# Kernel optimization log

Measured on AMD Instinct MI355X. Metric: run time of the kernel, lower is better.

Reference implementation:

```python
import jax, jax.numpy as jnp
import numpy as np

B, S, D = 8, 8192, 64
N_HASHES = 8
BUCKET_SIZE = 64
N_BUCKETS = S // BUCKET_SIZE  # 128
SELF_ATTN_VALUE = -5e4  # torch reformer TOKEN_SELF_ATTN_VALUE


def setup_inputs() -> dict:
    key = jax.random.key(0)
    k1, k2, k3 = jax.random.split(key, 3)
    qk = jax.random.normal(k1, (B, S, D), dtype=jnp.float32)
    v = jax.random.normal(k2, (B, S, D), dtype=jnp.float32)
    # LSH random rotations: (dim, n_hashes, n_buckets // 2), shared across batch/heads
    rotations = jax.random.normal(k3, (D, N_HASHES, N_BUCKETS // 2), dtype=jnp.float32)
    return {"qk": qk, "v": v, "rotations": rotations, "query_len": S}


def _look_one_back(x):
    # concatenate each chunk with the preceding chunk (wrapping) along the kv axis
    x_extra = jnp.concatenate([x[:, -1:], x[:, :-1]], axis=1)
    return jnp.concatenate([x, x_extra], axis=2)


def _lsh_bucketed_dots(qk, v, rotations):
    batch, seqlen, dim = qk.shape
    n_buckets = seqlen // BUCKET_SIZE
    # --- hash vectors: rotate, concat with negation, argmax -> bucket ids ---
    rotated = jnp.einsum('btf,fhi->bhti', qk, rotations)           # (B, H, S, nb/2)
    rotated = jnp.concatenate([rotated, -rotated], axis=-1)        # (B, H, S, nb)
    buckets = jnp.argmax(rotated, axis=-1)                         # (B, H, S) int
    offsets = (jnp.arange(N_HASHES) * n_buckets)[None, :, None]    # disjoint per round
    buckets = (buckets + offsets).reshape(batch, -1)               # (B, H*S)

    # --- stable bucket sort via composite key (all keys unique) ---
    ticker = jnp.arange(N_HASHES * seqlen)[None, :]                # (1, H*S)
    buckets_and_t = seqlen * buckets + (ticker % seqlen)
    sticker = jnp.argsort(buckets_and_t, axis=-1)                  # sort permutation
    undo_sort = jnp.argsort(sticker, axis=-1)                      # inverse permutation
    st = sticker % seqlen                                          # original token ids

    # --- gather tokens into bucket order ---
    sqk = jnp.take_along_axis(qk, st[..., None], axis=1)           # (B, H*S, D)
    sv = jnp.take_along_axis(v, st[..., None], axis=1)

    n_chunks = N_HASHES * n_buckets
    bq_t = st.reshape(batch, n_chunks, BUCKET_SIZE)                # (B, C, bs)
    bqk = sqk.reshape(batch, n_chunks, BUCKET_SIZE, dim)
    bv = sv.reshape(batch, n_chunks, BUCKET_SIZE, dim)

    bq = bqk
    bk = bqk / (jnp.linalg.norm(bqk, axis=-1, keepdims=True) + 1e-6)  # unit-length keys

    bk = _look_one_back(bk)       # (B, C, 2*bs, D)
    bv = _look_one_back(bv)
    bkv_t = _look_one_back(bq_t)  # (B, C, 2*bs)

    dots = jnp.einsum('buie,buje->buij', bq, bk) * (dim ** -0.5)   # (B, C, bs, 2*bs)
    self_mask = bq_t[:, :, :, None] == bkv_t[:, :, None, :]
    dots = jnp.where(self_mask, SELF_ATTN_VALUE, dots)
    return dots, undo_sort, bv


def reference(qk, v, rotations, query_len):
    batch, seqlen, dim = qk.shape
    dots, undo_sort, bv = _lsh_bucketed_dots(qk, v, rotations)
    dots_logsumexp = jax.nn.logsumexp(dots, axis=-1, keepdims=True)
    p = jnp.exp(dots - dots_logsumexp)                             # per-bucket softmax
    bo = jnp.einsum('buij,buje->buie', p, bv)                      # (B, C, bs, D)
    so = bo.reshape(batch, -1, dim)                                # (B, H*S, D)
    slogits = dots_logsumexp.reshape(batch, -1)                    # (B, H*S)
    # undo the bucket sort
    o = jnp.take_along_axis(so, undo_sort[..., None], axis=1)
    logits = jnp.take_along_axis(slogits, undo_sort, axis=1)
    o = o.reshape(batch, N_HASHES, seqlen, dim)[:, :, :query_len]
    logits = logits.reshape(batch, N_HASHES, seqlen, 1)[:, :, :query_len]
    # combine across hash rounds, weighted by per-round logsumexp
    probs = jnp.exp(logits - jax.nn.logsumexp(logits, axis=1, keepdims=True))
    out = jnp.sum(o * probs, axis=1)                               # (B, query_len, D)
    return out
```

## Files before the change

kernel.cpp:

```cpp
#include <hip/hip_runtime.h>
#include <math.h>

#define B_  8
#define S_  8192
#define D_  64
#define H_  8
#define NB_ 128
#define NC_ 1024
#define REP_CAP 65536
#define T2_ 2e-3f

typedef _Float16 f16x8 __attribute__((ext_vector_type(8)));
typedef _Float16 f16x2 __attribute__((ext_vector_type(2)));
typedef float    f32x4 __attribute__((ext_vector_type(4)));
typedef unsigned int uint_;

#define MFMA16(A, Bv, C) __builtin_amdgcn_mfma_f32_16x16x32_f16(A, Bv, C, 0, 0, 0)

__global__ __launch_bounds__(256) void rot_prep_kernel(
    const float* __restrict__ rot, _Float16* __restrict__ rotHi,
    _Float16* __restrict__ rotLo, float* __restrict__ rotT,
    int* __restrict__ cnt)
{
  __shared__ float rs[64 * 64];
  const int tid = threadIdx.x, h = blockIdx.x;
  if (h == 0 && tid == 0) *cnt = 0;
#pragma unroll
  for (int it = 0; it < 16; ++it) {
    const int f = it * 4 + (tid >> 6), i = tid & 63;
    rs[f * 64 + i] = rot[f * 512 + h * 64 + i];
  }
  __syncthreads();
  const int i = tid & 63, grp = tid >> 6;
  _Float16 hi[16], lo[16];
  float tf[16];
#pragma unroll
  for (int ff = 0; ff < 16; ++ff) {
    const float x = rs[(grp * 16 + ff) * 64 + i];
    tf[ff] = x;
    hi[ff] = (_Float16)x;
    lo[ff] = (_Float16)(x - (float)hi[ff]);
  }
  f16x8* dH = (f16x8*)(rotHi + h * 4096 + i * 64 + grp * 16);
  f16x8* dL = (f16x8*)(rotLo + h * 4096 + i * 64 + grp * 16);
  dH[0] = ((f16x8*)hi)[0]; dH[1] = ((f16x8*)hi)[1];
  dL[0] = ((f16x8*)lo)[0]; dL[1] = ((f16x8*)lo)[1];
  float4* dT = (float4*)(rotT + h * 4096 + i * 64 + grp * 16);
#pragma unroll
  for (int k = 0; k < 4; ++k) dT[k] = ((float4*)tf)[k];
}

__global__ __launch_bounds__(256) void hash_kernel(
    const float* __restrict__ qk, const float* __restrict__ v,
    const _Float16* __restrict__ rotHi, const _Float16* __restrict__ rotLo,
    _Float16* __restrict__ q16, _Float16* __restrict__ kn16,
    _Float16* __restrict__ v16,
    int* __restrict__ bucket, int* __restrict__ cnt, int2* __restrict__ list)
{
  __shared__ float rs[64 * 68];
  __shared__ _Float16 rH[64 * 72];
  __shared__ _Float16 rL[64 * 72];
  const int tid  = threadIdx.x;
  const int b    = blockIdx.x & 7;
  const int tile = blockIdx.x >> 3;
  const int lane = tid & 63, w = tid >> 6;
  const int m16  = lane & 15, qd = lane >> 4;

  {
    const int r = tid >> 2, qu = tid & 3;
    const int gt = b * S_ + tile * 64 + r;
    const size_t off = (size_t)gt * 64 + qu * 16;
    float x[16];
#pragma unroll
    for (int k = 0; k < 4; ++k) ((float4*)x)[k] = ((const float4*)(qk + off))[k];
#pragma unroll
    for (int k = 0; k < 4; ++k)
      *(float4*)(rs + r * 68 + qu * 16 + k * 4) = ((float4*)x)[k];
    float ss = 0.f;
#pragma unroll
    for (int k = 0; k < 16; ++k) ss = fmaf(x[k], x[k], ss);
    ss += __shfl_xor(ss, 1); ss += __shfl_xor(ss, 2);
    const float inv = 0.125f / (sqrtf(ss) + 1e-6f);
    f16x8 qh[2], kn[2];
#pragma unroll
    for (int j = 0; j < 16; ++j) {
      qh[j >> 3][j & 7] = (_Float16)x[j];
      kn[j >> 3][j & 7] = (_Float16)(x[j] * inv);
    }
    ((f16x8*)(q16  + off))[0] = qh[0]; ((f16x8*)(q16  + off))[1] = qh[1];
    ((f16x8*)(kn16 + off))[0] = kn[0]; ((f16x8*)(kn16 + off))[1] = kn[1];
    float y[16];
#pragma unroll
    for (int k = 0; k < 4; ++k) ((float4*)y)[k] = ((const float4*)(v + off))[k];
    f16x8 vv[2];
#pragma unroll
    for (int j = 0; j < 16; ++j) vv[j >> 3][j & 7] = (_Float16)y[j];
    ((f16x8*)(v16 + off))[0] = vv[0]; ((f16x8*)(v16 + off))[1] = vv[1];
  }
  __syncthreads();

  const int t = tile * 64 + w * 16 + m16;
  f16x8 BH0, BH1, BL0, BL1;
  {
    const float* srcl = rs + (w * 16 + m16) * 68 + 8 * qd;
    float x[16];
    ((float4*)x)[0] = *(const float4*)(srcl);
    ((float4*)x)[1] = *(const float4*)(srcl + 4);
    ((float4*)x)[2] = *(const float4*)(srcl + 32);
    ((float4*)x)[3] = *(const float4*)(srcl + 36);
#pragma unroll
    for (int j = 0; j < 8; ++j) {
      const _Float16 h0 = (_Float16)x[j];
      BH0[j] = h0; BL0[j] = (_Float16)(x[j] - (float)h0);
      const _Float16 h1 = (_Float16)x[j + 8];
      BH1[j] = h1; BL1[j] = (_Float16)(x[j + 8] - (float)h1);
    }
  }
  const int srow = tid >> 2, scol = (tid & 3) * 16;
  const uint_ qd16 = (uint_)(qd << 4);

  f16x8 cH0, cH1, cL0, cL1;
  {
    const _Float16* gH = rotHi + srow * 64 + scol;
    const _Float16* gL = rotLo + srow * 64 + scol;
    cH0 = ((const f16x8*)gH)[0]; cH1 = ((const f16x8*)gH)[1];
    cL0 = ((const f16x8*)gL)[0]; cL1 = ((const f16x8*)gL)[1];
  }

#pragma unroll 1
  for (int h = 0; h < 8; ++h) {
    __syncthreads();
    f16x8 nH0, nH1, nL0, nL1;
    if (h < 7) {
      const _Float16* gH = rotHi + (h + 1) * 4096 + srow * 64 + scol;
      const _Float16* gL = rotLo + (h + 1) * 4096 + srow * 64 + scol;
      nH0 = ((const f16x8*)gH)[0]; nH1 = ((const f16x8*)gH)[1];
      nL0 = ((const f16x8*)gL)[0]; nL1 = ((const f16x8*)gL)[1];
    }
    *(f16x8*)(rH + srow * 72 + scol)     = cH0;
    *(f16x8*)(rH + srow * 72 + scol + 8) = cH1;
    *(f16x8*)(rL + srow * 72 + scol)     = cL0;
    *(f16x8*)(rL + srow * 72 + scol + 8) = cL1;
    __syncthreads();

    f32x4 acc[4];
#pragma unroll
    for (int mt = 0; mt < 4; ++mt) acc[mt] = (f32x4){0.f, 0.f, 0.f, 0.f};
#pragma unroll
    for (int mt = 0; mt < 4; ++mt) {
      const _Float16* aH = rH + (16 * mt + m16) * 72 + 8 * qd;
      const _Float16* aL = rL + (16 * mt + m16) * 72 + 8 * qd;
      const f16x8 AH0 = *(const f16x8*)aH;
      const f16x8 AH1 = *(const f16x8*)(aH + 32);
      const f16x8 AL0 = *(const f16x8*)aL;
      const f16x8 AL1 = *(const f16x8*)(aL + 32);
      acc[mt] = MFMA16(AH0, BH0, acc[mt]);
      acc[mt] = MFMA16(AH1, BH1, acc[mt]);
      acc[mt] = MFMA16(AH0, BL0, acc[mt]);
      acc[mt] = MFMA16(AH1, BL1, acc[mt]);
      acc[mt] = MFMA16(AL0, BH0, acc[mt]);
      acc[mt] = MFMA16(AL1, BH1, acc[mt]);
    }

    float v1M = -1e30f, v2M = -1e30f, v1m = 1e30f, v2m = 1e30f;
#pragma unroll
    for (int mt = 0; mt < 4; ++mt)
#pragma unroll
      for (int rg = 0; rg < 4; ++rg) {
        uint_ u = __float_as_uint(acc[mt][rg]);
        u = (u & 0xFFFFFFC0u) | qd16 | (uint_)((mt << 2) | rg);
        const float xk = __uint_as_float(u);
        v2M = __builtin_amdgcn_fmed3f(v1M, v2M, xk);
        v1M = fmaxf(v1M, xk);
        v2m = __builtin_amdgcn_fmed3f(v1m, v2m, xk);
        v1m = fminf(v1m, xk);
      }
#pragma unroll
    for (int off = 16; off <= 32; off <<= 1) {
      const float o1M = __shfl_xor(v1M, off), o2M = __shfl_xor(v2M, off);
      v2M = __builtin_amdgcn_fmed3f(v1M, o1M, fmaxf(v2M, o2M));
      v1M = fmaxf(v1M, o1M);
      const float o1m = __shfl_xor(v1m, off), o2m = __shfl_xor(v2m, off);
      v2m = __builtin_amdgcn_fmed3f(v1m, o1m, fminf(v2m, o2m));
      v1m = fminf(v1m, o1m);
    }
    if (qd == 0) {
      const uint_ cM = __float_as_uint(v1M) & 63u;
      const uint_ cm = __float_as_uint(v1m) & 63u;
      const int ixM = 16 * (int)((cM >> 2) & 3u) + 4 * (int)(cM >> 4) + (int)(cM & 3u);
      const int ixm = 16 * (int)((cm >> 2) & 3u) + 4 * (int)(cm >> 4) + (int)(cm & 3u);
      const int bkt = (v1M >= -v1m) ? ixM : 64 + ixm;
      bucket[((size_t)(b * 8 + h)) * S_ + t] = bkt;
      const bool flag = ((v1M - v2M) < T2_) | ((v2m - v1m) < T2_) |
                        (fabsf(v1M + v1m) < T2_);
      if (flag) {
        const int s = atomicAdd(cnt, 1);
        if (s < REP_CAP) list[s] = make_int2(b * 8 + h, t);
      }
    }
    cH0 = nH0; cH1 = nH1; cL0 = nL0; cL1 = nL1;
  }
}

__global__ __launch_bounds__(256) void repair_kernel(
    const float* __restrict__ qk, const float* __restrict__ rotT,
    const int* __restrict__ cnt, const int2* __restrict__ list,
    int* __restrict__ bucket)
{
  const int n = min(*cnt, REP_CAP);
  const int lane = threadIdx.x & 63;
  const int wid  = (blockIdx.x * 256 + threadIdx.x) >> 6;
  const int nw   = gridDim.x * 4;
  for (int idx = wid; idx < n; idx += nw) {
    const int bh = list[idx].x, t = list[idx].y;
    const int b = bh >> 3, hh = bh & 7;
    const float* qrow = qk + ((size_t)b * S_ + t) * D_;
    const float* rcol = rotT + hh * 4096 + lane * 64;
    double acc = 0.0;
#pragma unroll
    for (int f0 = 0; f0 < 64; f0 += 4) {
      const float4 rq = *(const float4*)(qrow + f0);
      const float4 rc = *(const float4*)(rcol + f0);
      acc = fma((double)rq.x, (double)rc.x, acc);
      acc = fma((double)rq.y, (double)rc.y, acc);
      acc = fma((double)rq.z, (double)rc.z, acc);
      acc = fma((double)rq.w, (double)rc.w, acc);
    }
    double vM = acc; int iM = lane;
    double vm = acc; int im = lane;
#pragma unroll
    for (int off = 32; off >= 1; off >>= 1) {
      const double voM = __shfl_xor(vM, off); const int ioM = __shfl_xor(iM, off);
      if (voM > vM || (voM == vM && ioM < iM)) { vM = voM; iM = ioM; }
      const double vom = __shfl_xor(vm, off); const int iom = __shfl_xor(im, off);
      if (vom < vm || (vom == vm && iom < im)) { vm = vom; im = iom; }
    }
    if (lane == 0) {
      const int bkt = (vM >= -vm) ? iM : 64 + im;
      bucket[(size_t)bh * S_ + t] = bkt;
    }
  }
}

__global__ __launch_bounds__(1024) void sort_kernel(
    const int* __restrict__ bucket, int* __restrict__ st)
{
  __shared__ uint_ hist32[128 * 67];
  __shared__ unsigned short lb[S_];
  __shared__ int off[128];
  __shared__ int wtot;
  unsigned short* hist16 = (unsigned short*)hist32;
  const int tid = threadIdx.x;
  const int bh  = blockIdx.x;
  const size_t base = (size_t)bh * S_;
  const int lane = tid & 63;
  const unsigned long long ltmask = (1ull << lane) - 1ull;

#pragma unroll
  for (int k = 0; k < 9; ++k) {
    const int i = k * 1024 + tid;
    if (i < 128 * 67) hist32[i] = 0;
  }
  __syncthreads();

  int rl[8];
#pragma unroll
  for (int k = 0; k < 8; ++k) {
    const int t = k * 1024 + tid;
    const int bk = bucket[base + t];
    lb[t] = (unsigned short)bk;
    unsigned long long same = ~0ull;
#pragma unroll
    for (int bit = 0; bit < 7; ++bit) {
      const unsigned long long m = __ballot((bk >> bit) & 1);
      same &= ((bk >> bit) & 1) ? m : ~m;
    }
    rl[k] = __popcll(same & ltmask);
    if ((same & ltmask) == 0ull)
      hist16[bk * 134 + (t >> 6)] = (unsigned short)__popcll(same);
  }
  __syncthreads();

  int s = 0;
  if (tid < 128) {
    const uint_* row = hist32 + tid * 67;
#pragma unroll
    for (int g2 = 0; g2 < 64; ++g2) {
      const uint_ wv = row[g2];
      s += (int)((wv & 0xFFFFu) + (wv >> 16));
    }
  }
  int x = s;
#pragma unroll
  for (int d = 1; d < 64; d <<= 1) {
    const int y = __shfl_up(x, d);
    if (lane >= d) x += y;
  }
  if (tid == 63) wtot = x;
  __syncthreads();
  if (tid < 128) {
    if (tid >= 64) x += wtot;
    off[tid] = x - s;
  }
  __syncthreads();

  if (tid < 128) {
    int run = off[tid];
    unsigned short* rowp = hist16 + tid * 134;
#pragma unroll
    for (int g = 0; g < 128; ++g) {
      const int cg = rowp[g];
      rowp[g] = (unsigned short)run;
      run += cg;
    }
  }
  __syncthreads();

  const int b = bh >> 3, h = bh & 7;
  const size_t stb = (size_t)b * (H_ * S_) + (size_t)h * S_;
#pragma unroll
  for (int k = 0; k < 8; ++k) {
    const int t = k * 1024 + tid;
    const int bk = (int)lb[t];
    const int gb = (int)hist16[bk * 134 + (t >> 6)];
    st[stb + gb + rl[k]] = t;
  }
}

__global__ __launch_bounds__(256, 8) void attn_kernel(
    const _Float16* __restrict__ q16, const _Float16* __restrict__ kn16,
    const _Float16* __restrict__ v16, const int* __restrict__ st,
    _Float16* __restrict__ so, float* __restrict__ slog)
{
  __shared__ _Float16 smem[128 * 72];
  __shared__ __align__(16) int sIds[128];

  const int tid = threadIdx.x;
  const int b   = blockIdx.x & 7;
  const int c   = blockIdx.x >> 3;
  const int cm1 = (c + NC_ - 1) & (NC_ - 1);
  const size_t bst = (size_t)b * (H_ * S_);
  const size_t row0 = bst + (size_t)c * 64;
  const size_t row1 = bst + (size_t)cm1 * 64;

  const int lane = tid & 63;
  const int w    = tid >> 6;
  const int m16  = lane & 15;
  const int qd   = lane >> 4;

  if (tid < 128) sIds[tid] = (tid < 64) ? st[row0 + tid] : st[row1 + tid - 64];

  const int rid = st[row0 + 16 * w + m16];
  f16x8 q0, q1;
  {
    const _Float16* qp = q16 + ((size_t)b * S_ + rid) * 64 + 8 * qd;
    q0 = *(const f16x8*)qp;
    q1 = *(const f16x8*)(qp + 32);
  }

  const int r = tid >> 2, qu = tid & 3;
  {
    const int tokA = st[row0 + r];
    const int tokB = st[row1 + r];
    const f16x8* ska = (const f16x8*)(kn16 + ((size_t)b * S_ + tokA) * 64 + qu * 16);
    const f16x8* skb = (const f16x8*)(kn16 + ((size_t)b * S_ + tokB) * 64 + qu * 16);
    *(f16x8*)(smem + r * 72 + qu * 16)            = ska[0];
    *(f16x8*)(smem + r * 72 + qu * 16 + 8)        = ska[1];
    *(f16x8*)(smem + (64 + r) * 72 + qu * 16)     = skb[0];
    *(f16x8*)(smem + (64 + r) * 72 + qu * 16 + 8) = skb[1];
  }
  __syncthreads();

  f32x4 acc[8];
#pragma unroll
  for (int jt = 0; jt < 8; ++jt) acc[jt] = (f32x4){0.f, 0.f, 0.f, 0.f};

  __builtin_amdgcn_s_setprio(1);
#pragma unroll
  for (int jt = 0; jt < 8; ++jt) {
    const _Float16* krow = smem + (16 * jt + m16) * 72;
    const f16x8 kb0 = *(const f16x8*)(krow + 8 * qd);
    const f16x8 kb1 = *(const f16x8*)(krow + 32 + 8 * qd);
    acc[jt] = MFMA16(kb0, q0, acc[jt]);
    acc[jt] = MFMA16(kb1, q1, acc[jt]);
  }
  __builtin_amdgcn_s_setprio(0);

  float m = -1e30f;
#pragma unroll
  for (int jt = 0; jt < 8; ++jt) {
    const int4 cid = *(const int4*)(sIds + 16 * jt + 4 * qd);
    float x;
    x = acc[jt][0]; if (cid.x == rid) x = -5e4f; acc[jt][0] = x; m = fmaxf(m, x);
    x = acc[jt][1]; if (cid.y == rid) x = -5e4f; acc[jt][1] = x; m = fmaxf(m, x);
    x = acc[jt][2]; if (cid.z == rid) x = -5e4f; acc[jt][2] = x; m = fmaxf(m, x);
    x = acc[jt][3]; if (cid.w == rid) x = -5e4f; acc[jt][3] = x; m = fmaxf(m, x);
  }
  m = fmaxf(m, __shfl_xor(m, 16));
  m = fmaxf(m, __shfl_xor(m, 32));
  float sum = 0.f;
#pragma unroll
  for (int jt = 0; jt < 8; ++jt)
#pragma unroll
    for (int rg = 0; rg < 4; ++rg) {
      const float e = __expf(acc[jt][rg] - m);
      acc[jt][rg] = e;
      sum += e;
    }
  sum += __shfl_xor(sum, 16);
  sum += __shfl_xor(sum, 32);
  const float rinv = 1.f / sum;

  const int hh = c >> 7;
  const size_t hb = ((size_t)(b * 8 + hh)) * S_;
  if (qd == 0) slog[hb + rid] = m + __logf(sum);

  f16x8 pa[4];
#pragma unroll
  for (int s = 0; s < 4; ++s)
#pragma unroll
    for (int j = 0; j < 8; ++j)
      pa[s][j] = (_Float16)acc[2 * s + (j >> 2)][j & 3];

  const int c0 = 2 * r;
  const int k0 = 32 * (c0 >> 5) + 16 * ((c0 >> 2) & 1) + 4 * ((c0 >> 3) & 3) + (c0 & 3);
  const int tok0 = sIds[k0], tok1 = sIds[k0 + 1];
  f16x8 va[2], vb[2];
  {
    const f16x8* s0 = (const f16x8*)(v16 + ((size_t)b * S_ + tok0) * 64 + qu * 16);
    const f16x8* s1 = (const f16x8*)(v16 + ((size_t)b * S_ + tok1) * 64 + qu * 16);
    va[0] = s0[0]; va[1] = s0[1];
    vb[0] = s1[0]; vb[1] = s1[1];
  }
  __syncthreads();

  {
    const int swz = (qu << 3) ^ ((qu & 1) << 5);
    _Float16* dst = smem + (c0 ^ swz);
#pragma unroll
    for (int jj = 0; jj < 16; ++jj) {
      const int d = 16 * qu + jj;
      f16x2 pk; pk[0] = va[jj >> 3][jj & 7]; pk[1] = vb[jj >> 3][jj & 7];
      *(f16x2*)(dst + d * 136) = pk;
    }
  }
  __syncthreads();

  f32x4 oacc[4];
#pragma unroll
  for (int dt = 0; dt < 4; ++dt) oacc[dt] = (f32x4){0.f, 0.f, 0.f, 0.f};
  __builtin_amdgcn_s_setprio(1);
#pragma unroll
  for (int s = 0; s < 4; ++s) {
#pragma unroll
    for (int dt = 0; dt < 4; ++dt) {
      const _Float16* vp = smem + (16 * dt + m16) * 136
                         + 32 * (s ^ (dt & 1)) + 8 * (qd ^ dt);
      const f16x8 bv = *(const f16x8*)(vp);
      oacc[dt] = MFMA16(pa[s], bv, oacc[dt]);
    }
  }
  __builtin_amdgcn_s_setprio(0);

  float rin[4];
#pragma unroll
  for (int rg = 0; rg < 4; ++rg) rin[rg] = __shfl(rinv, 4 * qd + rg);

  __syncthreads();
#pragma unroll
  for (int dt = 0; dt < 4; ++dt)
#pragma unroll
    for (int rg = 0; rg < 4; ++rg)
      smem[(16 * w + 4 * qd + rg) * 72 + 16 * dt + m16] =
          (_Float16)(oacc[dt][rg] * rin[rg]);
  __syncthreads();

  {
    const int tok = sIds[r];
    const f16x8* srcp = (const f16x8*)(smem + r * 72 + qu * 16);
    const f16x8 o0 = srcp[0], o1 = srcp[1];
    f16x8* dstp = (f16x8*)(so + (hb + tok) * 64 + qu * 16);
    dstp[0] = o0; dstp[1] = o1;
  }
}

__global__ __launch_bounds__(256) void combine_kernel(
    const _Float16* __restrict__ so, const float* __restrict__ slog,
    float* __restrict__ out)
{
  const int blk = blockIdx.x;
  const int b   = blk & 7;
  const int t   = (blk >> 3) * 32 + (threadIdx.x >> 3);
  const int oct = threadIdx.x & 7;
  const size_t base8 = (size_t)(b * 8) * S_ + t;

  float l[8];
#pragma unroll
  for (int h = 0; h < 8; ++h) l[h] = slog[base8 + (size_t)h * S_];
  float m = l[0];
#pragma unroll
  for (int h = 1; h < 8; ++h) m = fmaxf(m, l[h]);
  float wv[8], W = 0.f;
#pragma unroll
  for (int h = 0; h < 8; ++h) { wv[h] = expf(l[h] - m); W += wv[h]; }
  const float iW = 1.f / W;

  float acc[8] = {0.f, 0.f, 0.f, 0.f, 0.f, 0.f, 0.f, 0.f};
#pragma unroll
  for (int h = 0; h < 8; ++h) {
    const f16x8 vv = *(const f16x8*)(so + (base8 + (size_t)h * S_) * 64 + oct * 8);
#pragma unroll
    for (int j = 0; j < 8; ++j) acc[j] = fmaf(wv[h], (float)vv[j], acc[j]);
  }
  float4 o0, o1;
  o0.x = acc[0] * iW; o0.y = acc[1] * iW; o0.z = acc[2] * iW; o0.w = acc[3] * iW;
  o1.x = acc[4] * iW; o1.y = acc[5] * iW; o1.z = acc[6] * iW; o1.w = acc[7] * iW;
  float4* dst = (float4*)(out + ((size_t)b * S_ + t) * 64 + oct * 8);
  dst[0] = o0; dst[1] = o1;
}

extern "C" void kernel_launch(void* const* d_in, const int* in_sizes, int n_in,
                              void* d_out, int out_size, void* d_ws, size_t ws_size,
                              hipStream_t stream)
{
  const float* qk  = (const float*)d_in[0];
  const float* v   = (const float*)d_in[1];
  const float* rot = (const float*)d_in[2];
  float* out = (float*)d_out;

  char* ws = (char*)d_ws;
  const size_t MB = 1ull << 20, KB = 1024;
  int*      bucket = (int*)      (ws + 0 * MB);
  int*      st     = (int*)      (ws + 2 * MB);
  float*    slog   = (float*)    (ws + 4 * MB);
  _Float16* q16    = (_Float16*) (ws + 8 * MB);
  _Float16* kn16   = (_Float16*) (ws + 16 * MB);
  _Float16* v16    = (_Float16*) (ws + 24 * MB);
  _Float16* rotHi  = (_Float16*) (ws + 32 * MB);
  _Float16* rotLo  = (_Float16*) (ws + 32 * MB + 64 * KB);
  int*      cnt    = (int*)      (ws + 32 * MB + 128 * KB);
  int2*     list   = (int2*)     (ws + 32 * MB + 192 * KB);
  float*    rotT   = (float*)    (ws + 32 * MB + 768 * KB);
  _Float16* so     = (_Float16*) (ws + 33 * MB);
  if (ws_size < 98 * MB) return;

  hipLaunchKernelGGL(rot_prep_kernel, dim3(8),         dim3(256),  0, stream,
                     rot, rotHi, rotLo, rotT, cnt);
  hipLaunchKernelGGL(hash_kernel,     dim3(8 * 128),   dim3(256),  0, stream,
                     qk, v, rotHi, rotLo, q16, kn16, v16, bucket, cnt, list);
  hipLaunchKernelGGL(repair_kernel,   dim3(256),       dim3(256),  0, stream,
                     qk, rotT, cnt, list, bucket);
  hipLaunchKernelGGL(sort_kernel,     dim3(64),        dim3(1024), 0, stream,
                     bucket, st);
  hipLaunchKernelGGL(attn_kernel,     dim3(B_ * NC_),  dim3(256),  0, stream,
                     q16, kn16, v16, st, so, slog);
  hipLaunchKernelGGL(combine_kernel,  dim3(B_ * S_ * 8 / 256), dim3(256), 0, stream,
                     so, slog, out);
}
```

Baseline: 177.6 us.

## Fuse bucket repair into sort kernel and rework attention output stores

Removes the separate repair kernel launch. Each sort block now scans the flagged-token list, picks out the entries for its own (batch, hash) row, and recomputes those buckets in double precision before sorting. The attention kernel's scatter of outputs to the sorted buffer now uses 8 threads per row over two halves with nontemporal 16-byte stores. The fused scan makes every one of the 64 sort blocks read the whole list serially and adds work at the start of sort, in exchange for one fewer launch.

Result: slower. 215.4 us (+21.3%).

```diff
diff --git a/kernel.cpp b/kernel.cpp
--- a/kernel.cpp
+++ b/kernel.cpp
@@ -202,48 +202,10 @@
   }
 }
 
-__global__ __launch_bounds__(256) void repair_kernel(
+__global__ __launch_bounds__(1024) void sort_kernel(
     const float* __restrict__ qk, const float* __restrict__ rotT,
     const int* __restrict__ cnt, const int2* __restrict__ list,
-    int* __restrict__ bucket)
-{
-  const int n = min(*cnt, REP_CAP);
-  const int lane = threadIdx.x & 63;
-  const int wid  = (blockIdx.x * 256 + threadIdx.x) >> 6;
-  const int nw   = gridDim.x * 4;
-  for (int idx = wid; idx < n; idx += nw) {
-    const int bh = list[idx].x, t = list[idx].y;
-    const int b = bh >> 3, hh = bh & 7;
-    const float* qrow = qk + ((size_t)b * S_ + t) * D_;
-    const float* rcol = rotT + hh * 4096 + lane * 64;
-    double acc = 0.0;
-#pragma unroll
-    for (int f0 = 0; f0 < 64; f0 += 4) {
-      const float4 rq = *(const float4*)(qrow + f0);
-      const float4 rc = *(const float4*)(rcol + f0);
-      acc = fma((double)rq.x, (double)rc.x, acc);
-      acc = fma((double)rq.y, (double)rc.y, acc);
-      acc = fma((double)rq.z, (double)rc.z, acc);
-      acc = fma((double)rq.w, (double)rc.w, acc);
-    }
-    double vM = acc; int iM = lane;
-    double vm = acc; int im = lane;
-#pragma unroll
-    for (int off = 32; off >= 1; off >>= 1) {
-      const double voM = __shfl_xor(vM, off); const int ioM = __shfl_xor(iM, off);
-      if (voM > vM || (voM == vM && ioM < iM)) { vM = voM; iM = ioM; }
-      const double vom = __shfl_xor(vm, off); const int iom = __shfl_xor(im, off);
-      if (vom < vm || (vom == vm && iom < im)) { vm = vom; im = iom; }
-    }
-    if (lane == 0) {
-      const int bkt = (vM >= -vm) ? iM : 64 + im;
-      bucket[(size_t)bh * S_ + t] = bkt;
-    }
-  }
-}
-
-__global__ __launch_bounds__(1024) void sort_kernel(
-    const int* __restrict__ bucket, int* __restrict__ st)
+    int* __restrict__ bucket, int* __restrict__ st)
 {
   __shared__ uint_ hist32[128 * 67];
   __shared__ unsigned short lb[S_];
@@ -256,6 +218,50 @@
   const int lane = tid & 63;
   const unsigned long long ltmask = (1ull << lane) - 1ull;
 
+  {
+    const int n = min(*cnt, REP_CAP);
+    const int b = bh >> 3, hh = bh & 7;
+    for (int base_i = 0; base_i < n; base_i += 1024) {
+      const int idx = base_i + tid;
+      int match = 0, ty = 0;
+      if (idx < n) {
+        const int2 e = list[idx];
+        ty = e.y;
+        match = (e.x == bh);
+      }
+      unsigned long long mm = __ballot(match);
+      while (mm) {
+        const int src = (int)__builtin_ctzll(mm); mm &= mm - 1;
+        const int t = __shfl(ty, src);
+        const float* qrow = qk + ((size_t)b * S_ + t) * D_;
+        const float* rcol = rotT + hh * 4096 + lane * 64;
+        double acc = 0.0;
+#pragma unroll
+        for (int f0 = 0; f0 < 64; f0 += 4) {
+          const float4 rq = *(const float4*)(qrow + f0);
+          const float4 rc = *(const float4*)(rcol + f0);
+          acc = fma((double)rq.x, (double)rc.x, acc);
+          acc = fma((double)rq.y, (double)rc.y, acc);
+          acc = fma((double)rq.z, (double)rc.z, acc);
+          acc = fma((double)rq.w, (double)rc.w, acc);
+        }
+        double vM = acc; int iM = lane;
+        double vm = acc; int im = lane;
+#pragma unroll
+        for (int o = 32; o >= 1; o >>= 1) {
+          const double voM = __shfl_xor(vM, o); const int ioM = __shfl_xor(iM, o);
+          if (voM > vM || (voM == vM && ioM < iM)) { vM = voM; iM = ioM; }
+          const double vom = __shfl_xor(vm, o); const int iom = __shfl_xor(im, o);
+          if (vom < vm || (vom == vm && iom < im)) { vm = vom; im = iom; }
+        }
+        if (lane == 0) {
+          const int bkt = (vM >= -vm) ? iM : 64 + im;
+          bucket[(size_t)bh * S_ + t] = bkt;
+        }
+      }
+    }
+  }
+
 #pragma unroll
   for (int k = 0; k < 9; ++k) {
     const int i = k * 1024 + tid;
@@ -476,11 +482,14 @@
   __syncthreads();
 
   {
-    const int tok = sIds[r];
-    const f16x8* srcp = (const f16x8*)(smem + r * 72 + qu * 16);
-    const f16x8 o0 = srcp[0], o1 = srcp[1];
-    f16x8* dstp = (f16x8*)(so + (hb + tok) * 64 + qu * 16);
-    dstp[0] = o0; dstp[1] = o1;
+    const int seg = tid & 7;
+#pragma unroll
+    for (int half = 0; half < 2; ++half) {
+      const int r2 = half * 32 + (tid >> 3);
+      const int tok = sIds[r2];
+      const f16x8 ov = *(const f16x8*)(smem + r2 * 72 + seg * 8);
+      __builtin_nontemporal_store(ov, (f16x8*)(so + (hb + tok) * 64 + seg * 8));
+    }
   }
 }
 
@@ -548,10 +557,8 @@
                      rot, rotHi, rotLo, rotT, cnt);
   hipLaunchKernelGGL(hash_kernel,     dim3(8 * 128),   dim3(256),  0, stream,
                      qk, v, rotHi, rotLo, q16, kn16, v16, bucket, cnt, list);
-  hipLaunchKernelGGL(repair_kernel,   dim3(256),       dim3(256),  0, stream,
-                     qk, rotT, cnt, list, bucket);
   hipLaunchKernelGGL(sort_kernel,     dim3(64),        dim3(1024), 0, stream,
-                     bucket, st);
+                     qk, rotT, cnt, list, bucket, st);
   hipLaunchKernelGGL(attn_kernel,     dim3(B_ * NC_),  dim3(256),  0, stream,
                      q16, kn16, v16, st, so, slog);
   hipLaunchKernelGGL(combine_kernel,  dim3(B_ * S_ * 8 / 256), dim3(256), 0, stream,
```
